# Kernel optimization log

Hardware: AMD Instinct MI355X
Metric: run time of the kernel (lower is better)

The kernel has to match this reference:

```python
import jax, jax.numpy as jnp
import numpy as np

RADIUS = 2  # matches init kwarg

def lga3d(cost, filters, radius):
    """One pass of GANet local guided 3D aggregation.
    cost:    [B, C, D, H, W]
    filters: [B, 3*K*K, H, W], K = 2*radius+1; 3 groups for depth offsets d-1, d, d+1.
    Out-of-range taps (depth or spatial) contribute zero.
    """
    B, C, D, H, W = cost.shape
    K = 2 * radius + 1
    # zero-pad: 1 plane on each side of depth, `radius` on each spatial side
    cp = jnp.pad(cost, ((0, 0), (0, 0), (1, 1), (radius, radius), (radius, radius)))
    out = jnp.zeros_like(cost)
    for g in range(3):            # depth offsets -1, 0, +1
        for i in range(K):        # vertical window offset
            for j in range(K):    # horizontal window offset
                w = filters[:, g * K * K + i * K + j][:, None, None]  # [B,1,1,H,W]
                patch = jax.lax.dynamic_slice(cp, (0, 0, g, i, j), (B, C, D, H, W))
                out = out + w * patch
    return out


def setup_inputs() -> dict:
    key = jax.random.key(0)
    k1, k2 = jax.random.split(key)
    B, C, D, H, W = 1, 16, 48, 128, 256
    K = 2 * RADIUS + 1
    cost = jax.random.normal(k1, (B, C, D, H, W), dtype=jnp.float32)
    filters = jax.random.normal(k2, (B, 3 * K * K, H, W), dtype=jnp.float32) * 0.1
    return {"cost": cost, "filters": filters}


def reference(cost, filters):
    # Lga3d3Function applies the aggregation three times with the same filters.
    out = lga3d(cost, filters, RADIUS)
    out = lga3d(out, filters, RADIUS)
    out = lga3d(out, filters, RADIUS)
    return out
```

## Files before the change

kernel.cpp:

```cpp
#include <hip/hip_runtime.h>


namespace {
constexpr int C  = 16, D = 48, H = 128, W = 256;
constexpr int TH = 4, TW = 64;
constexpr int LH = TH + 4;
constexpr int LW = 72;
constexpr int NF = 75;
constexpr int HW = H * W;
constexpr int SLOTS = LH * (LW / 4);
}

__global__ __launch_bounds__(256, 4)
void lga_pass(const float* __restrict__ in, const float* __restrict__ filt,
              float* __restrict__ out)
{
    __shared__ float buf[2][LH * LW];

    const int tx = threadIdx.x;
    const int ty = threadIdx.y;
    const int tid = ty * 64 + tx;
    const int w0 = blockIdx.x * TW;
    const int h0 = blockIdx.y * TH;
    const int c  = blockIdx.z;
    const int h  = h0 + ty;
    const int w  = w0 + tx;

    float f[NF];
    #pragma unroll
    for (int k = 0; k < NF; ++k)
        f[k] = filt[k * HW + h * W + w];

    const bool haveSlot = tid < SLOTS;
    const int r  = tid / 18;
    const int q  = tid - r * 18;
    const int gh = h0 - 2 + r;
    const int gw = w0 - 4 + 4 * q;
    const bool valid = haveSlot && (gh >= 0) && (gh < H) && (gw >= 0) && (gw < W);
    const int planeOff = gh * W + gw;
    const int ldsOff   = r * LW + 4 * q;
    const float* planeBase = in + c * (D * HW);

    auto stage = [&](int dp, int bsel) {
        float4 v = make_float4(0.f, 0.f, 0.f, 0.f);
        if (valid) v = *(const float4*)(planeBase + dp * HW + planeOff);
        if (haveSlot) *(float4*)(&buf[bsel][ldsOff]) = v;
    };

    stage(0, 0);
    __syncthreads();

    float a_prev = 0.f, a_cur = 0.f;
    float* outp = out + c * (D * HW) + h * W + w;

    for (int d = 0; d < D; ++d) {
        if (d + 1 < D) stage(d + 1, (d + 1) & 1);

        const float* bp = &buf[d & 1][ty * LW + tx + 2];
        float s0 = 0.f, s1 = 0.f, s2 = 0.f;
        #pragma unroll
        for (int i = 0; i < 5; ++i) {
            #pragma unroll
            for (int j = 0; j < 5; ++j) {
                float v = bp[i * LW + j];
                s0 = fmaf(f[     i * 5 + j], v, s0);
                s1 = fmaf(f[25 + i * 5 + j], v, s1);
                s2 = fmaf(f[50 + i * 5 + j], v, s2);
            }
        }

        float done = a_prev + s2;
        if (d > 0) outp[(d - 1) * HW] = done;
        a_prev = a_cur + s1;
        a_cur  = s0;
        __syncthreads();
    }
    outp[(D - 1) * HW] = a_prev;
}

extern "C" void kernel_launch(void* const* d_in, const int* in_sizes, int n_in,
                              void* d_out, int out_size, void* d_ws, size_t ws_size,
                              hipStream_t stream)
{
    const float* cost = (const float*)d_in[0];
    const float* filt = (const float*)d_in[1];
    float* out = (float*)d_out;

    const size_t needBytes = (size_t)C * D * HW * sizeof(float);
    float* tmp = (ws_size >= needBytes) ? (float*)d_ws : (float*)d_in[0];

    dim3 block(64, 4, 1);
    dim3 grid(W / TW, H / TH, C);

    lga_pass<<<grid, block, 0, stream>>>(cost, filt, out);
    lga_pass<<<grid, block, 0, stream>>>(out,  filt, tmp);
    lga_pass<<<grid, block, 0, stream>>>(tmp,  filt, out);
}
```

Measured before the change: 418.9 us.

## Process four channels per block to reuse register-held filter taps

Each block now handles four channels at once and stores them interleaved as float4 in LDS, so the 75 per-pixel filter values loaded into registers are reused across four channels instead of being reloaded per channel. The tile width halves to 32, the block shrinks to 128 threads, and the grid's channel dimension shrinks by four. Staging now uses scalar strided global loads (one per channel) instead of a float4 row load, and each thread holds four times the accumulators, which raises register pressure and lowers occupancy. An empty asm barrier pins the filters in registers.

Result: slower. 446.2 us (+6.5%).

```diff
diff --git a/kernel.cpp b/kernel.cpp
--- a/kernel.cpp
+++ b/kernel.cpp
@@ -3,94 +3,128 @@
 
 namespace {
 constexpr int C  = 16, D = 48, H = 128, W = 256;
-constexpr int TH = 4, TW = 64;
+constexpr int NC = 4;
+constexpr int TH = 4, TW = 32;
 constexpr int LH = TH + 4;
-constexpr int LW = 72;
+constexpr int LW = TW + 8;
+constexpr int HW = H * W;
+constexpr int DHW = D * HW;
 constexpr int NF = 75;
-constexpr int HW = H * W;
-constexpr int SLOTS = LH * (LW / 4);
+constexpr int CELLS = LH * LW;
 }
 
-__global__ __launch_bounds__(256, 4)
+__global__ __launch_bounds__(128, 2)
 void lga_pass(const float* __restrict__ in, const float* __restrict__ filt,
               float* __restrict__ out)
 {
-    __shared__ float buf[2][LH * LW];
+    __shared__ float4 buf[2][CELLS];
 
-    const int tx = threadIdx.x;
-    const int ty = threadIdx.y;
-    const int tid = ty * 64 + tx;
-    const int w0 = blockIdx.x * TW;
-    const int h0 = blockIdx.y * TH;
-    const int c  = blockIdx.z;
-    const int h  = h0 + ty;
-    const int w  = w0 + tx;
+    const int tx  = threadIdx.x;
+    const int ty  = threadIdx.y;
+    const int tid = ty * 32 + tx;
+    const int w0  = blockIdx.x * TW;
+    const int h0  = blockIdx.y * TH;
+    const int c0  = blockIdx.z * NC;
+    const int h   = h0 + ty;
+    const int w   = w0 + tx;
 
     float f[NF];
     #pragma unroll
     for (int k = 0; k < NF; ++k)
         f[k] = filt[k * HW + h * W + w];
+    #pragma unroll
+    for (int k = 0; k < NF; ++k)
+        asm volatile("" : "+v"(f[k]));
 
-    const bool haveSlot = tid < SLOTS;
-    const int r  = tid / 18;
-    const int q  = tid - r * 18;
-    const int gh = h0 - 2 + r;
-    const int gw = w0 - 4 + 4 * q;
-    const bool valid = haveSlot && (gh >= 0) && (gh < H) && (gw >= 0) && (gw < W);
-    const int planeOff = gh * W + gw;
-    const int ldsOff   = r * LW + 4 * q;
-    const float* planeBase = in + c * (D * HW);
+    const float* base = in + (size_t)c0 * DHW;
 
-    auto stage = [&](int dp, int bsel) {
-        float4 v = make_float4(0.f, 0.f, 0.f, 0.f);
-        if (valid) v = *(const float4*)(planeBase + dp * HW + planeOff);
-        if (haveSlot) *(float4*)(&buf[bsel][ldsOff]) = v;
+    auto stage = [&](int p, int bsel) {
+        #pragma unroll
+        for (int k = 0; k < 3; ++k) {
+            int cell = tid + k * 128;
+            if (cell < CELLS) {
+                int r   = cell / LW;
+                int col = cell - r * LW;
+                int gh  = h0 - 2 + r;
+                int gw  = w0 - 4 + col;
+                float4 v = make_float4(0.f, 0.f, 0.f, 0.f);
+                if (gh >= 0 && gh < H && gw >= 0 && gw < W) {
+                    const float* pb = base + (size_t)p * HW + gh * W + gw;
+                    v.x = pb[0];
+                    v.y = pb[DHW];
+                    v.z = pb[2 * DHW];
+                    v.w = pb[3 * DHW];
+                }
+                buf[bsel][cell] = v;
+            }
+        }
     };
 
     stage(0, 0);
     __syncthreads();
 
-    float a_prev = 0.f, a_cur = 0.f;
-    float* outp = out + c * (D * HW) + h * W + w;
+    float4 a_prev = make_float4(0.f, 0.f, 0.f, 0.f);
+    float4 a_cur  = make_float4(0.f, 0.f, 0.f, 0.f);
+    float* op0 = out + (size_t)c0 * DHW + h * W + w;
 
     for (int d = 0; d < D; ++d) {
         if (d + 1 < D) stage(d + 1, (d + 1) & 1);
 
-        const float* bp = &buf[d & 1][ty * LW + tx + 2];
-        float s0 = 0.f, s1 = 0.f, s2 = 0.f;
+        const float4* bp = &buf[d & 1][ty * LW + tx + 2];
+        float4 s0 = make_float4(0.f, 0.f, 0.f, 0.f);
+        float4 s1 = s0, s2 = s0;
         #pragma unroll
         for (int i = 0; i < 5; ++i) {
             #pragma unroll
             for (int j = 0; j < 5; ++j) {
-                float v = bp[i * LW + j];
-                s0 = fmaf(f[     i * 5 + j], v, s0);
-                s1 = fmaf(f[25 + i * 5 + j], v, s1);
-                s2 = fmaf(f[50 + i * 5 + j], v, s2);
+                float4 v = bp[i * LW + j];
+                float F0 = f[     i * 5 + j];
+                float F1 = f[25 + i * 5 + j];
+                float F2 = f[50 + i * 5 + j];
+                s0.x = fmaf(F0, v.x, s0.x); s0.y = fmaf(F0, v.y, s0.y);
+                s0.z = fmaf(F0, v.z, s0.z); s0.w = fmaf(F0, v.w, s0.w);
+                s1.x = fmaf(F1, v.x, s1.x); s1.y = fmaf(F1, v.y, s1.y);
+                s1.z = fmaf(F1, v.z, s1.z); s1.w = fmaf(F1, v.w, s1.w);
+                s2.x = fmaf(F2, v.x, s2.x); s2.y = fmaf(F2, v.y, s2.y);
+                s2.z = fmaf(F2, v.z, s2.z); s2.w = fmaf(F2, v.w, s2.w);
             }
         }
 
-        float done = a_prev + s2;
-        if (d > 0) outp[(d - 1) * HW] = done;
-        a_prev = a_cur + s1;
-        a_cur  = s0;
+        if (d > 0) {
+            float* op = op0 + (size_t)(d - 1) * HW;
+            op[0]       = a_prev.x + s2.x;
+            op[DHW]     = a_prev.y + s2.y;
+            op[2 * DHW] = a_prev.z + s2.z;
+            op[3 * DHW] = a_prev.w + s2.w;
+        }
+        a_prev.x = a_cur.x + s1.x; a_prev.y = a_cur.y + s1.y;
+        a_prev.z = a_cur.z + s1.z; a_prev.w = a_cur.w + s1.w;
+        a_cur = s0;
         __syncthreads();
     }
-    outp[(D - 1) * HW] = a_prev;
+    {
+        float* op = op0 + (size_t)(D - 1) * HW;
+        op[0]       = a_prev.x;
+        op[DHW]     = a_prev.y;
+        op[2 * DHW] = a_prev.z;
+        op[3 * DHW] = a_prev.w;
+    }
 }
 
 extern "C" void kernel_launch(void* const* d_in, const int* in_sizes, int n_in,
                               void* d_out, int out_size, void* d_ws, size_t ws_size,
                               hipStream_t stream)
 {
+    (void)in_sizes; (void)n_in; (void)out_size;
     const float* cost = (const float*)d_in[0];
     const float* filt = (const float*)d_in[1];
     float* out = (float*)d_out;
 
-    const size_t needBytes = (size_t)C * D * HW * sizeof(float);
+    const size_t needBytes = (size_t)C * DHW * sizeof(float);
     float* tmp = (ws_size >= needBytes) ? (float*)d_ws : (float*)d_in[0];
 
-    dim3 block(64, 4, 1);
-    dim3 grid(W / TW, H / TH, C);
+    dim3 block(32, 4, 1);
+    dim3 grid(W / TW, H / TH, C / NC);
 
     lga_pass<<<grid, block, 0, stream>>>(cost, filt, out);
     lga_pass<<<grid, block, 0, stream>>>(out,  filt, tmp);
```
